# Kernel tuning notes

Hardware: AMD Instinct MI355X
Metric: run time of the kernel (lower is better)

Reference implementation:

```python
import jax, jax.numpy as jnp
import numpy as np

LEVELS = 9
NLPOW = 1.4
BORDER_INV = 0.9
MIN_SHAPE = 5
PATCH = 4
EPS = 1e-8


def shift2(x, dy, dx):
    # out[..., u, v] = x[..., u - dy, v - dx], zero padded
    H, W = x.shape[-2], x.shape[-1]
    pad = [(0, 0)] * (x.ndim - 2) + [(max(dy, 0), max(-dy, 0)), (max(dx, 0), max(-dx, 0))]
    xp = jnp.pad(x, pad)
    return xp[..., max(-dy, 0):max(-dy, 0) + H, max(-dx, 0):max(-dx, 0) + W]


def maxpool2(x):
    # F.max_pool2d(x, 3, padding=1, stride=2) over the last two (target-image) dims
    return jax.lax.reduce_window(x, jnp.array(-jnp.inf, x.dtype), jax.lax.max,
                                 (1, 1, 3, 3), (1, 1, 2, 2),
                                 [(0, 0), (0, 0), (1, 1), (1, 1)])


def activation(c):
    # corr.clamp_(min=0).pow_(nlpow)
    return jnp.maximum(c, 0.0) ** NLPOW


def first_level(desc1, desc2):
    C, H1, W1 = desc1.shape[1:]
    H2, W2 = desc2.shape[2:]
    p = PATCH
    # F.unfold(desc1, 4, stride=4): non-overlapping 4x4 patches, row-major over (H1//4, W1//4)
    patches = desc1[0].reshape(C, H1 // p, p, W1 // p, p).transpose(1, 3, 0, 2, 4)
    patches = patches.reshape(-1, C, p, p)                       # (N, C, 4, 4)
    # normalized cross-correlation of every patch with desc2, padding 2 -> (H2+1, W2+1)
    num = jax.lax.conv_general_dilated(desc2, patches, (1, 1), [(2, 2), (2, 2)])  # (1, N, H2+1, W2+1)
    pnorm = jnp.sqrt(jnp.sum(patches ** 2, axis=(1, 2, 3)))      # (N,) patch norms
    sq = jnp.sum(desc2 ** 2, axis=1, keepdims=True)              # (1, 1, H2, W2)
    ones = jnp.ones((1, 1, p, p), desc2.dtype)
    wnorm = jnp.sqrt(jax.lax.conv_general_dilated(sq, ones, (1, 1), [(2, 2), (2, 2)]))
    corr = num / (pnorm[None, :, None, None] * wnorm + EPS)
    corr = corr.reshape(H1 // p, W1 // p, H2 + 1, W2 + 1)
    weights = (pnorm > 0).astype(corr.dtype).reshape(H1 // p, W1 // p)
    return corr, weights


def sparse_conv_fwd(corr, weights):
    # DeepMatching-style 2x2 children aggregation with validity weights.
    # corr: (H1, W1, h, w); weights: (H1, W1). Parent grid is ceil-halved.
    H1, W1 = corr.shape[:2]
    Hp, Wp = -(-H1 // 2), -(-W1 // 2)
    corr = jnp.pad(corr, [(0, 2 * Hp - H1), (0, 2 * Wp - W1), (0, 0), (0, 0)])
    weights = jnp.pad(weights, [(0, 2 * Hp - H1), (0, 2 * Wp - W1)])
    num = 0.0
    den = 0.0
    for di in (0, 1):
        for dj in (0, 1):
            w = weights[di::2, dj::2]
            num = num + w[..., None, None] * shift2(corr[di::2, dj::2], 2 * di - 1, 2 * dj - 1)
            den = den + w
    # border_inv normalization: interior patches divide by 4, borders by >= 4*0.9
    out = num / jnp.maximum(den, 4.0 * BORDER_INV)[..., None, None]
    return out, den * 0.25


def sparse_conv_rev(upper):
    # reverse aggregation: scatter parent maps back to the 2x2 children with inverse shifts
    Hp, Wp, hp, wp = upper.shape
    out = jnp.zeros((2 * Hp, 2 * Wp, hp, wp), upper.dtype)
    for di in (0, 1):
        for dj in (0, 1):
            out = out.at[di::2, dj::2].set(shift2(upper, 1 - 2 * di, 1 - 2 * dj))
    return out


def max_unpool(up, lower):
    # route parent scores back to the argmax locations of the 3x3/stride-2 max-pool of `lower`
    mp = maxpool2(lower)                                  # (H1, W1, hp, wp)
    h, w = lower.shape[-2:]
    ui = jnp.minimum(jnp.arange(h) // 2, mp.shape[-2] - 1)
    vi = jnp.minimum(jnp.arange(w) // 2, mp.shape[-1] - 1)
    up_mp = mp[..., ui[:, None], vi[None, :]]             # pooled max broadcast to full res
    up_val = up[..., ui[:, None], vi[None, :]]            # parent value broadcast to full res
    return jnp.where(lower == up_mp, jnp.maximum(lower, up_val), lower)


def pump_forward(desc1, desc2):
    corr, weights = first_level(desc1, desc2)
    pyramid = [activation(corr)]
    for level in range(1, LEVELS + 1):
        pooled = maxpool2(pyramid[-1])
        upper, weights = sparse_conv_fwd(pooled, weights)
        pyramid.append(activation(upper))
        if min(upper.shape[-2:]) <= MIN_SHAPE:
            break
    for level in range(len(pyramid) - 1, 0, -1):
        lo = pyramid[level - 1]
        rev = sparse_conv_rev(pyramid[level])[:lo.shape[0], :lo.shape[1]]
        pyramid[level - 1] = max_unpool(rev, lo)
        pyramid.pop()
    return pyramid[0]


def setup_inputs():
    key = jax.random.key(0)
    k1, k2 = jax.random.split(key)
    C, H, W = 128, 128, 128
    desc1 = jax.random.normal(k1, (1, C, H, W), jnp.float32)
    desc2 = jax.random.normal(k2, (1, C, H, W), jnp.float32)
    # PUMP pixel descriptors are L2-normalized per pixel
    desc1 = desc1 / (jnp.linalg.norm(desc1, axis=1, keepdims=True) + 1e-8)
    desc2 = desc2 / (jnp.linalg.norm(desc2, axis=1, keepdims=True) + 1e-8)
    return {"desc1": desc1, "desc2": desc2}


def reference(desc1, desc2):
    # refined full-resolution 4D correlation volume (H1//4, W1//4, H2+1, W2+1)
    return pump_forward(desc1, desc2)
```

## Files before the change

### kernel.cpp

```cpp
#include <hip/hip_runtime.h>
#include <hip/hip_fp16.h>
#include <math.h>

typedef unsigned int uint;
typedef unsigned short ushort;
typedef short f16x8 __attribute__((ext_vector_type(8)));
typedef float f32x4 __attribute__((ext_vector_type(4)));

#define NLPOW 1.4f
#define EPSF 1e-8f
#define HO 129

__device__ __forceinline__ float activate(float c) {
    c = fmaxf(c, 0.0f);
    return powf(c, NLPOW);
}

__device__ __forceinline__ void f16split(float v, ushort& h, ushort& l) {
    __half hv = __float2half(v);
    h = __half_as_ushort(hv);
    float r = (v - __half2float(hv)) * 2048.0f;
    l = __half_as_ushort(__float2half(r));
}

__device__ __forceinline__ void gld_lds16(const ushort* g, ushort* l) {
    __builtin_amdgcn_global_load_lds(
        (const __attribute__((address_space(1))) void*)g,
        (__attribute__((address_space(3))) void*)l,
        16, 0, 0);
}

__global__ void prep_d2(const float* __restrict__ d2, ushort* __restrict__ d2p) {
    int idx = blockIdx.x * 256 + threadIdx.x;
    if (idx >= 140 * 148 * 128) return;
    int c = idx & 127;
    int xp = (idx >> 7) % 148;
    int yp = idx / (148 * 128);
    int y = yp - 2, x = xp - 2;
    float v = 0.f;
    if ((unsigned)y < 128u && (unsigned)x < 128u)
        v = d2[c * 16384 + y * 128 + x];
    ushort h, lo;
    f16split(v, h, lo);
    long o = ((long)(yp * 148 + xp)) * 256 + c;
    d2p[o] = h;
    d2p[o + 128] = lo;
}

__global__ void build_Afrag(const float* __restrict__ d1, ushort* __restrict__ Ag) {
    int idx = blockIdx.x * 256 + threadIdx.x;
    if (idx >= 8 * 64 * 2 * 128 * 40) return;
    int kk = idx % 40;
    int row = (idx / 40) % 128;
    int pl = (idx / 5120) % 2;
    int s = (idx / 10240) % 64;
    int mb = idx / 655360;
    ushort hv = 0, lv = 0;
    if (kk < 32) {
        int kp = s * 32 + kk;
        int c = kp & 127;
        int ab = kp >> 7;
        int a = ab >> 2, b = ab & 3;
        int p = mb * 128 + row;
        int i = p >> 5, j = p & 31;
        float v = d1[c * 16384 + (4 * i + a) * 128 + (4 * j + b)];
        f16split(v, hv, lv);
    }
    Ag[idx] = pl ? lv : hv;
}

__global__ void pnorm_k(const float* __restrict__ d1, float* __restrict__ pn) {
    int p = blockIdx.x;
    int t = threadIdx.x;
    int i = p >> 5, j = p & 31;
    int pix = t & 15;
    int a = pix >> 2, b = pix & 3;
    int cg = t >> 4;
    const float* base = d1 + (4 * i + a) * 128 + (4 * j + b);
    float s = 0.f;
    for (int c = cg * 32; c < cg * 32 + 32; ++c) {
        float v = base[c * 16384];
        s += v * v;
    }
    #pragma unroll
    for (int off = 32; off > 0; off >>= 1) s += __shfl_down(s, off);
    if (t == 0) pn[p] = sqrtf(s);
}

__global__ void sq_k(const float* __restrict__ d2, float* __restrict__ sq) {
    int idx = blockIdx.x * 256 + threadIdx.x;
    if (idx >= 16384) return;
    float s = 0.f;
    for (int c = 0; c < 128; ++c) {
        float v = d2[c * 16384 + idx];
        s += v * v;
    }
    sq[idx] = s;
}

__global__ void wnorm_k(const float* __restrict__ sq, float* __restrict__ wnorm) {
    int idx = blockIdx.x * 256 + threadIdx.x;
    if (idx >= HO * HO) return;
    int y = idx / HO, x = idx % HO;
    float s = 0.f;
    #pragma unroll
    for (int a = 0; a < 4; ++a) {
        int yy = y - 2 + a;
        if ((unsigned)yy >= 128u) continue;
        #pragma unroll
        for (int b = 0; b < 4; ++b) {
            int xx = x - 2 + b;
            if ((unsigned)xx >= 128u) continue;
            s += sq[yy * 128 + xx];
        }
    }
    wnorm[idx] = sqrtf(s);
}

__global__ __launch_bounds__(256, 2) void conv_mfma(
    const ushort* __restrict__ Ag,
    const ushort* __restrict__ d2p,
    const float* __restrict__ pn, const float* __restrict__ wnorm,
    float* __restrict__ out)
{
    __shared__ __align__(16) ushort A2[2][2][5120];

    const int t = threadIdx.x;
    const int mb = blockIdx.x & 7;
    const int nb = blockIdx.x >> 3;
    const int ny0 = (nb / 9) * 8;
    const int nx0 = (nb % 9) * 16;
    const int p0 = mb * 128;

    const int l = t & 63;
    const int w = t >> 6;
    const int wm = w & 1, wn_ = w >> 1;
    const int lm = l & 15, lg = l >> 4;

    f32x4 accH[4][4] = {};
    f32x4 accX[4][4] = {};

    const ushort* aSrcT = Ag + (long)mb * 64 * 10240 + t * 8;
    ushort* aDstT = &A2[0][0][0] + t * 8;
    const ushort* aBase = &A2[0][0][0] + (wm * 64 + lm) * 40 + lg * 8;

    const ushort* bNi[4];
    #pragma unroll
    for (int ni = 0; ni < 4; ++ni)
        bNi[ni] = d2p + ((long)(ny0 + wn_ * 4 + ni) * 148 + (nx0 + lm)) * 256 + lg * 8;

    uint4 B0[8], B1[8];

    auto stageA = [&](int s, int cur) {
        const ushort* src = aSrcT + (long)s * 10240;
        ushort* dst = aDstT + cur * 10240;
        #pragma unroll
        for (int i = 0; i < 5; ++i)
            gld_lds16(src + i * 2048, dst + i * 2048);
    };
    auto loadB = [&](int s, uint4 (&B)[8]) {
        const int ab = s >> 2;
        const int uoff = ((ab >> 2) * 148 + (ab & 3)) * 256 + (s & 3) * 32;
        #pragma unroll
        for (int ni = 0; ni < 4; ++ni) {
            const ushort* p = bNi[ni] + uoff;
            B[ni * 2 + 0] = *(const uint4*)p;
            B[ni * 2 + 1] = *(const uint4*)(p + 128);
        }
    };
    auto mfmaStep = [&](int cur, const uint4 (&B)[8]) {
        f16x8 fah[4], fal[4];
        #pragma unroll
        for (int mi = 0; mi < 4; ++mi) {
            fah[mi] = *(const f16x8*)(aBase + cur * 10240 + mi * 640);
            fal[mi] = *(const f16x8*)(aBase + cur * 10240 + 5120 + mi * 640);
        }
        #pragma unroll
        for (int ni = 0; ni < 4; ++ni) {
            f16x8 fbh = *(const f16x8*)&B[ni * 2 + 0];
            f16x8 fbl = *(const f16x8*)&B[ni * 2 + 1];
            #pragma unroll
            for (int mi = 0; mi < 4; ++mi) {
                accH[mi][ni] = __builtin_amdgcn_mfma_f32_16x16x32_f16(fah[mi], fbh, accH[mi][ni], 0, 0, 0);
                accX[mi][ni] = __builtin_amdgcn_mfma_f32_16x16x32_f16(fah[mi], fbl, accX[mi][ni], 0, 0, 0);
                accX[mi][ni] = __builtin_amdgcn_mfma_f32_16x16x32_f16(fal[mi], fbh, accX[mi][ni], 0, 0, 0);
            }
        }
    };

    stageA(0, 0);
    loadB(0, B0);
    __syncthreads();

    for (int s = 0; s < 64; s += 2) {
        if (s < 63) { stageA(s + 1, 1); loadB(s + 1, B1); }
        mfmaStep(0, B0);
        __syncthreads();

        if (s < 62) { stageA(s + 2, 0); loadB(s + 2, B0); }
        mfmaStep(1, B1);
        __syncthreads();
    }

    #pragma unroll
    for (int mi = 0; mi < 4; ++mi) {
        #pragma unroll
        for (int ni = 0; ni < 4; ++ni) {
            int y = ny0 + wn_ * 4 + ni;
            int x = nx0 + lm;
            if (y < HO && x < HO) {
                float wv = wnorm[y * HO + x];
                f32x4 vh = accH[mi][ni];
                f32x4 vx = accX[mi][ni];
                #pragma unroll
                for (int r = 0; r < 4; ++r) {
                    int p = p0 + wm * 64 + mi * 16 + lg * 4 + r;
                    float num = vh[r] + vx[r] * (1.0f / 2048.0f);
                    float c = num / (pn[p] * wv + EPSF);
                    out[(long)p * (HO * HO) + y * HO + x] = activate(c);
                }
            }
        }
    }
}

__device__ __forceinline__ void maxpool_body(const float* __restrict__ in,
                                             float* __restrict__ out,
                                             int idx, int h, int hp) {
    int s = idx % hp;
    int r = (idx / hp) % hp;
    int g = idx / (hp * hp);
    const float* base = in + (long)g * h * h;
    int y0 = 2 * r - 1, x0 = 2 * s - 1;
    float m = -1e30f;
    #pragma unroll
    for (int dy = 0; dy < 3; ++dy) {
        int y = y0 + dy;
        if ((unsigned)y >= (unsigned)h) continue;
        #pragma unroll
        for (int dx = 0; dx < 3; ++dx) {
            int x = x0 + dx;
            if ((unsigned)x >= (unsigned)h) continue;
            m = fmaxf(m, base[y * h + x]);
        }
    }
    out[idx] = m;
}

__device__ __forceinline__ void sparse_body(const float* __restrict__ pooled,
                                            float* __restrict__ out,
                                            int idx, int G2, int h) {
    int x = idx % h;
    int y = (idx / h) % h;
    int J = (idx / (h * h)) % G2;
    int I = idx / (h * h * G2);
    int G = 2 * G2;
    float s = 0.f;
    #pragma unroll
    for (int di = 0; di < 2; ++di) {
        int yy = y + 1 - 2 * di;
        if ((unsigned)yy >= (unsigned)h) continue;
        #pragma unroll
        for (int dj = 0; dj < 2; ++dj) {
            int xx = x + 1 - 2 * dj;
            if ((unsigned)xx >= (unsigned)h) continue;
            s += pooled[((((2 * I + di) * G) + (2 * J + dj)) * (long)h + yy) * h + xx];
        }
    }
    out[idx] = activate(0.25f * s);
}

__device__ __forceinline__ void unpool_body(float* __restrict__ lo,
                                            const float* __restrict__ pooled,
                                            const float* __restrict__ up,
                                            int idx, int G, int hl, int hp) {
    int x = idx % hl;
    int y = (idx / hl) % hl;
    int gj = (idx / (hl * hl)) % G;
    int gi = idx / (hl * hl * G);
    float l = lo[idx];
    float m = pooled[(((long)gi * G + gj) * hp + (y >> 1)) * hp + (x >> 1)];
    if (l == m) {
        int ry = (y >> 1) - 1 + 2 * (gi & 1);
        int rx = (x >> 1) - 1 + 2 * (gj & 1);
        float uv = 0.f;
        if ((unsigned)ry < (unsigned)hp && (unsigned)rx < (unsigned)hp)
            uv = up[((((long)(gi >> 1)) * (G >> 1) + (gj >> 1)) * hp + ry) * hp + rx];
        lo[idx] = fmaxf(l, uv);
    }
}

__global__ void maxpool_k(const float* __restrict__ in, float* __restrict__ out,
                          int GG, int h, int hp) {
    int idx = blockIdx.x * 256 + threadIdx.x;
    if (idx >= GG * hp * hp) return;
    maxpool_body(in, out, idx, h, hp);
}

__global__ void sparse_fwd_k(const float* __restrict__ pooled, float* __restrict__ out,
                             int G2, int h) {
    int idx = blockIdx.x * 256 + threadIdx.x;
    if (idx >= G2 * G2 * h * h) return;
    sparse_body(pooled, out, idx, G2, h);
}

__global__ void unpool_k(float* __restrict__ lo, const float* __restrict__ pooled,
                         const float* __restrict__ up, int G, int hl, int hp) {
    int idx = blockIdx.x * 256 + threadIdx.x;
    if (idx >= G * G * hl * hl) return;
    unpool_body(lo, pooled, up, idx, G, hl, hp);
}

__global__ void small_levels(float* __restrict__ pyr2,
                             float* __restrict__ pool3, float* __restrict__ pyr3,
                             float* __restrict__ pool4, float* __restrict__ pyr4,
                             float* __restrict__ pool5, float* __restrict__ pyr5)
{
    const int t = threadIdx.x;
    for (int i = t; i < 64 * 17 * 17; i += 1024) maxpool_body(pyr2, pool3, i, 33, 17);
    __syncthreads();
    for (int i = t; i < 16 * 17 * 17; i += 1024) sparse_body(pool3, pyr3, i, 4, 17);
    __syncthreads();
    for (int i = t; i < 16 * 9 * 9; i += 1024) maxpool_body(pyr3, pool4, i, 17, 9);
    __syncthreads();
    for (int i = t; i < 4 * 9 * 9; i += 1024) sparse_body(pool4, pyr4, i, 2, 9);
    __syncthreads();
    for (int i = t; i < 4 * 5 * 5; i += 1024) maxpool_body(pyr4, pool5, i, 9, 5);
    __syncthreads();
    for (int i = t; i < 5 * 5; i += 1024) sparse_body(pool5, pyr5, i, 1, 5);
    __syncthreads();
    for (int i = t; i < 4 * 9 * 9; i += 1024) unpool_body(pyr4, pool5, pyr5, i, 2, 9, 5);
    __syncthreads();
    for (int i = t; i < 16 * 17 * 17; i += 1024) unpool_body(pyr3, pool4, pyr4, i, 4, 17, 9);
    __syncthreads();
    for (int i = t; i < 64 * 33 * 33; i += 1024) unpool_body(pyr2, pool3, pyr3, i, 8, 33, 17);
}

#define PN_OFF    0L
#define WN_OFF    1024L
#define SQ_OFF    17728L
#define CBASE     34112L
#define D2P_OFF   (CBASE)
#define AG_OFF    (CBASE + 2652160L)
#define POOL1_OFF (CBASE)
#define PYR1_OFF  (CBASE + 4326400L)
#define POOL2_OFF (CBASE + 5408000L)
#define PYR2_OFF  (CBASE + 5686784L)
#define POOL3_OFF (CBASE + 5756480L)
#define PYR3_OFF  (CBASE + 5774976L)
#define POOL4_OFF (CBASE + 5779600L)
#define PYR4_OFF  (CBASE + 5780896L)
#define POOL5_OFF (CBASE + 5781220L)
#define PYR5_OFF  (CBASE + 5781320L)

extern "C" void kernel_launch(void* const* d_in, const int* in_sizes, int n_in,
                              void* d_out, int out_size, void* d_ws, size_t ws_size,
                              hipStream_t stream) {
    const float* d1 = (const float*)d_in[0];
    const float* d2 = (const float*)d_in[1];
    float* out = (float*)d_out;
    float* ws = (float*)d_ws;

    float* pnf   = ws + PN_OFF;
    float* wnf   = ws + WN_OFF;
    float* sqf   = ws + SQ_OFF;
    ushort* d2p  = (ushort*)(ws + D2P_OFF);
    ushort* Ag   = (ushort*)(ws + AG_OFF);
    float* pool1 = ws + POOL1_OFF;
    float* pyr1  = ws + PYR1_OFF;
    float* pool2 = ws + POOL2_OFF;
    float* pyr2  = ws + PYR2_OFF;
    float* pool3 = ws + POOL3_OFF;
    float* pyr3  = ws + PYR3_OFF;
    float* pool4 = ws + POOL4_OFF;
    float* pyr4  = ws + PYR4_OFF;
    float* pool5 = ws + POOL5_OFF;
    float* pyr5  = ws + PYR5_OFF;

    prep_d2<<<(140 * 148 * 128 + 255) / 256, 256, 0, stream>>>(d2, d2p);
    build_Afrag<<<(8 * 64 * 2 * 128 * 40 + 255) / 256, 256, 0, stream>>>(d1, Ag);
    pnorm_k<<<1024, 64, 0, stream>>>(d1, pnf);
    sq_k<<<64, 256, 0, stream>>>(d2, sqf);
    wnorm_k<<<(HO * HO + 255) / 256, 256, 0, stream>>>(sqf, wnf);

    conv_mfma<<<8 * 153, 256, 0, stream>>>(Ag, d2p, pnf, wnf, out);

    maxpool_k<<<(1024 * 65 * 65 + 255) / 256, 256, 0, stream>>>(out, pool1, 1024, 129, 65);
    sparse_fwd_k<<<(256 * 65 * 65 + 255) / 256, 256, 0, stream>>>(pool1, pyr1, 16, 65);
    maxpool_k<<<(256 * 33 * 33 + 255) / 256, 256, 0, stream>>>(pyr1, pool2, 256, 65, 33);
    sparse_fwd_k<<<(64 * 33 * 33 + 255) / 256, 256, 0, stream>>>(pool2, pyr2, 8, 33);

    small_levels<<<1, 1024, 0, stream>>>(pyr2, pool3, pyr3, pool4, pyr4, pool5, pyr5);

    unpool_k<<<(256 * 4225 + 255) / 256, 256, 0, stream>>>(pyr1, pool2, pyr2, 16, 65, 33);
    unpool_k<<<(1024 * 16641 + 255) / 256, 256, 0, stream>>>(out, pool1, pyr1, 32, 129, 65);
}
```

Baseline: 691.1 us.

## Stage B tiles through LDS with single buffering and raise occupancy to three blocks

The conv MFMA kernel now stages the desc2 (B) operand into shared memory using direct global-to-LDS loads instead of holding it in registers. The A/B shared buffers drop from double to single buffering, so each k-step computes, syncs, loads the next stage and syncs again. Launch bounds rise to three blocks per SM to recover latency hiding through occupancy. The trade-off is losing the software prefetch overlap and adding an extra barrier per iteration. In exchange, register pressure falls and B reads can be shared through LDS.

Result: slower. 785.6 us (+13.7%).

```diff
diff --git a/kernel.cpp b/kernel.cpp
--- a/kernel.cpp
+++ b/kernel.cpp
@@ -117,13 +117,14 @@
     wnorm[idx] = sqrtf(s);
 }
 
-__global__ __launch_bounds__(256, 2) void conv_mfma(
+__global__ __launch_bounds__(256, 3) void conv_mfma(
     const ushort* __restrict__ Ag,
     const ushort* __restrict__ d2p,
     const float* __restrict__ pn, const float* __restrict__ wnorm,
     float* __restrict__ out)
 {
-    __shared__ __align__(16) ushort A2[2][2][5120];
+    __shared__ __align__(16) ushort A1[2][5120];
+    __shared__ __align__(16) ushort B1[2][5120];
 
     const int t = threadIdx.x;
     const int mb = blockIdx.x & 7;
@@ -141,44 +142,50 @@
     f32x4 accX[4][4] = {};
 
     const ushort* aSrcT = Ag + (long)mb * 64 * 10240 + t * 8;
-    ushort* aDstT = &A2[0][0][0] + t * 8;
-    const ushort* aBase = &A2[0][0][0] + (wm * 64 + lm) * 40 + lg * 8;
-
-    const ushort* bNi[4];
-    #pragma unroll
-    for (int ni = 0; ni < 4; ++ni)
-        bNi[ni] = d2p + ((long)(ny0 + wn_ * 4 + ni) * 148 + (nx0 + lm)) * 256 + lg * 8;
-
-    uint4 B0[8], B1[8];
-
-    auto stageA = [&](int s, int cur) {
-        const ushort* src = aSrcT + (long)s * 10240;
-        ushort* dst = aDstT + cur * 10240;
+    ushort* aDstT = &A1[0][0] + t * 8;
+    ushort* bDstT = &B1[0][0] + t * 8;
+    uint bOff[5];
+    #pragma unroll
+    for (int i = 0; i < 5; ++i) {
+        int byte = i * 4096 + t * 16;
+        int plane = byte / 10240;
+        int rem = byte % 10240;
+        int row = rem / 80;
+        int off = rem % 80;
+        bOff[i] = (off < 64)
+            ? (uint)(((ny0 + (row >> 4)) * 148 + (nx0 + (row & 15))) * 256 + plane * 128 + off / 2)
+            : 0u;
+    }
+
+    const ushort* aBase = &A1[0][0] + (wm * 64 + lm) * 40 + lg * 8;
+    const ushort* bBase = &B1[0][0] + (wn_ * 64 + lm) * 40 + lg * 8;
+
+    auto stage = [&](int s) {
+        const ushort* aS = aSrcT + (long)s * 10240;
         #pragma unroll
         for (int i = 0; i < 5; ++i)
-            gld_lds16(src + i * 2048, dst + i * 2048);
+            gld_lds16(aS + i * 2048, aDstT + i * 2048);
+        const int ab = s >> 2;
+        const uint uoff = ((ab >> 2) * 148 + (ab & 3)) * 256 + (s & 3) * 32;
+        #pragma unroll
+        for (int i = 0; i < 5; ++i)
+            gld_lds16(d2p + bOff[i] + uoff, bDstT + i * 2048);
     };
-    auto loadB = [&](int s, uint4 (&B)[8]) {
-        const int ab = s >> 2;
-        const int uoff = ((ab >> 2) * 148 + (ab & 3)) * 256 + (s & 3) * 32;
+
+    stage(0);
+    __syncthreads();
+
+    for (int s = 0; s < 64; ++s) {
+        f16x8 fah[4], fal[4];
+        #pragma unroll
+        for (int mi = 0; mi < 4; ++mi) {
+            fah[mi] = *(const f16x8*)(aBase + mi * 640);
+            fal[mi] = *(const f16x8*)(aBase + 5120 + mi * 640);
+        }
         #pragma unroll
         for (int ni = 0; ni < 4; ++ni) {
-            const ushort* p = bNi[ni] + uoff;
-            B[ni * 2 + 0] = *(const uint4*)p;
-            B[ni * 2 + 1] = *(const uint4*)(p + 128);
-        }
-    };
-    auto mfmaStep = [&](int cur, const uint4 (&B)[8]) {
-        f16x8 fah[4], fal[4];
-        #pragma unroll
-        for (int mi = 0; mi < 4; ++mi) {
-            fah[mi] = *(const f16x8*)(aBase + cur * 10240 + mi * 640);
-            fal[mi] = *(const f16x8*)(aBase + cur * 10240 + 5120 + mi * 640);
-        }
-        #pragma unroll
-        for (int ni = 0; ni < 4; ++ni) {
-            f16x8 fbh = *(const f16x8*)&B[ni * 2 + 0];
-            f16x8 fbl = *(const f16x8*)&B[ni * 2 + 1];
+            f16x8 fbh = *(const f16x8*)(bBase + ni * 640);
+            f16x8 fbl = *(const f16x8*)(bBase + 5120 + ni * 640);
             #pragma unroll
             for (int mi = 0; mi < 4; ++mi) {
                 accH[mi][ni] = __builtin_amdgcn_mfma_f32_16x16x32_f16(fah[mi], fbh, accH[mi][ni], 0, 0, 0);
@@ -186,19 +193,8 @@
                 accX[mi][ni] = __builtin_amdgcn_mfma_f32_16x16x32_f16(fal[mi], fbh, accX[mi][ni], 0, 0, 0);
             }
         }
-    };
-
-    stageA(0, 0);
-    loadB(0, B0);
-    __syncthreads();
-
-    for (int s = 0; s < 64; s += 2) {
-        if (s < 63) { stageA(s + 1, 1); loadB(s + 1, B1); }
-        mfmaStep(0, B0);
         __syncthreads();
-
-        if (s < 62) { stageA(s + 2, 0); loadB(s + 2, B0); }
-        mfmaStep(1, B1);
+        if (s < 63) stage(s + 1);
         __syncthreads();
     }
 
```
